# Kernel tuning notes

Hardware: AMD Instinct MI355X
Metric: run time of the kernel (lower is better)

## Reference

```python
import jax, jax.numpy as jnp
import numpy as np

N_NODES = 50000
N_EDGES = 800000
IN_DIM = 128
HID_DIM = 128
OUT_DIM = 128


def setup_inputs() -> dict:
    key = jax.random.key(0)
    k = jax.random.split(key, 8)
    x = jax.random.normal(k[0], (N_NODES, IN_DIM), dtype=jnp.float32)
    edge_index = jax.random.randint(k[1], (2, N_EDGES), 0, N_NODES, dtype=jnp.int64)
    edge_weight = jax.random.uniform(k[2], (N_EDGES,), dtype=jnp.float32)
    # GCNConv params: weight [in, out] (glorot-ish), bias [out]
    W1 = jax.random.normal(k[3], (IN_DIM, HID_DIM), dtype=jnp.float32) / np.sqrt(IN_DIM)
    b1 = jnp.zeros((HID_DIM,), dtype=jnp.float32)
    W2 = jax.random.normal(k[4], (HID_DIM, OUT_DIM), dtype=jnp.float32) / np.sqrt(HID_DIM)
    b2 = jnp.zeros((OUT_DIM,), dtype=jnp.float32)
    return {"x": x, "edge_index": edge_index, "edge_weight": edge_weight,
            "W1": W1, "b1": b1, "W2": W2, "b2": b2}


def gcn_conv(x, W, b, src, dst, ew, n_nodes):
    """PyG GCNConv: add self-loops (weight 1), symmetric D^-1/2 (A+I) D^-1/2 norm."""
    h = x @ W  # [N, out]
    deg = jax.ops.segment_sum(ew, dst, num_segments=n_nodes) + 1.0  # +1 for self loop
    dis = jnp.where(deg > 0, jax.lax.rsqrt(deg), 0.0)  # deg^{-1/2}
    norm = dis[src] * ew * dis[dst]  # [E]
    msg = h[src] * norm[:, None]  # gather + weight -> [E, out]
    agg = jax.ops.segment_sum(msg, dst, num_segments=n_nodes)
    # self-loop contribution: norm_ii = dis[i] * 1 * dis[i]
    agg = agg + h * (dis * dis)[:, None]
    return agg + b


def reference(x, edge_index, edge_weight, W1, b1, W2, b2):
    src, dst = edge_index[0], edge_index[1]
    n = x.shape[0]
    h = gcn_conv(x, W1, b1, src, dst, edge_weight, n)
    h = jax.nn.relu(h)
    out = gcn_conv(h, W2, b2, src, dst, edge_weight, n)
    return out
```

## Files before the change

### kernel.cpp

```cpp
#include <hip/hip_runtime.h>

#define NDIM 128
#define NPART 8

typedef __attribute__((ext_vector_type(8))) short bf16x8;
typedef __attribute__((ext_vector_type(4))) float floatx4;

__device__ __forceinline__ float bflo(unsigned v){ return __uint_as_float(v << 16); }
__device__ __forceinline__ float bfhi(unsigned v){ return __uint_as_float(v & 0xffff0000u); }
__device__ __forceinline__ unsigned f2bf(float f){
  unsigned u = __float_as_uint(f);
  return (u + 0x7fffu + ((u >> 16) & 1u)) >> 16;
}

__global__ void k_prep0(unsigned long long* __restrict__ pk,
                        const float* __restrict__ W1, const float* __restrict__ W2,
                        unsigned short* __restrict__ Wp1, unsigned short* __restrict__ Wp2,
                        int n){
  int i = blockIdx.x * 256 + threadIdx.x;
  if (i < n) pk[i] = 0ULL;
  if (i < NDIM * NDIM){
    int k = i >> 7, c = i & 127;
    int kt = k >> 5, kq = (k >> 3) & 3, j = k & 7;
    int Lb = kq * 16 + (c & 15);
    int idx = (((kt * 8 + (c >> 4)) * 64) + Lb) * 8 + j;
    Wp1[idx] = (unsigned short)f2bf(W1[i]);
    Wp2[idx] = (unsigned short)f2bf(W2[i]);
  }
}

__global__ void k_deg(const int* __restrict__ ei, const float* __restrict__ ew,
                      unsigned long long* pk, unsigned short* __restrict__ rank, int E){
  int e = blockIdx.x * blockDim.x + threadIdx.x;
  if (e >= E) return;
  int d = ei[E + e];
  unsigned fx = (unsigned)__float2uint_rn(ew[e] * 1048576.0f);
  unsigned long long old = atomicAdd(&pk[d], (1ULL << 44) | (unsigned long long)fx);
  rank[e] = (unsigned short)(old >> 44);
}

__global__ __launch_bounds__(1024) void k_scan1(const unsigned long long* __restrict__ pk,
                                                int* __restrict__ off,
                                                int* __restrict__ bsum, int n){
  __shared__ int wsum[16];
  int t = threadIdx.x;
  int i = blockIdx.x * 1024 + t;
  int c = (i < n) ? (int)(pk[i] >> 44) : 0;
  int lane = t & 63, w = t >> 6;
  int v = c;
  #pragma unroll
  for (int d = 1; d < 64; d <<= 1){ int u = __shfl_up(v, d); if (lane >= d) v += u; }
  if (lane == 63) wsum[w] = v;
  __syncthreads();
  if (w == 0){
    int sv = (lane < 16) ? wsum[lane] : 0;
    #pragma unroll
    for (int d = 1; d < 16; d <<= 1){ int u = __shfl_up(sv, d); if (lane >= d) sv += u; }
    if (lane < 16) wsum[lane] = sv;
  }
  __syncthreads();
  int base = (w > 0) ? wsum[w - 1] : 0;
  if (i < n) off[i] = base + v - c;
  if (t == 1023) bsum[blockIdx.x] = wsum[15];
}

__global__ __launch_bounds__(1024) void k_scan23(int* __restrict__ off,
                                                 const int* __restrict__ bsum,
                                                 const unsigned long long* __restrict__ pk,
                                                 float* __restrict__ dis, int n, int E, int nb){
  __shared__ int sBase;
  int t = threadIdx.x;
  if (t < 64){
    int c2 = (t < nb) ? bsum[t] : 0;
    int v2 = c2;
    #pragma unroll
    for (int d = 1; d < 64; d <<= 1){ int u = __shfl_up(v2, d); if (t >= d) v2 += u; }
    if (t == (int)blockIdx.x) sBase = v2 - c2;
  }
  __syncthreads();
  int i = blockIdx.x * 1024 + t;
  if (i == 0) off[n] = E;
  if (i >= n) return;
  off[i] += sBase;
  float deg = 1.0f + (float)(pk[i] & ((1ULL << 44) - 1)) * (1.0f / 1048576.0f);
  dis[i] = rsqrtf(deg);
}

__global__ __launch_bounds__(256) void k_place(const int* __restrict__ ei,
                                               const float* __restrict__ ew,
                                               const unsigned short* __restrict__ rank,
                                               const float* __restrict__ dis,
                                               const int* __restrict__ off,
                                               unsigned* __restrict__ edges,
                                               int E, int N){
  int pid = blockIdx.x % NPART;
  int cid = blockIdx.x / NPART;
  int C   = gridDim.x / NPART;
  int per = (E + C - 1) / C;
  int e0 = cid * per;
  int e1 = min(e0 + per, E);
  int lo = (int)(((long long)pid * N) / NPART);
  int hi = (int)(((long long)(pid + 1) * N) / NPART);
  for (int e = e0 + threadIdx.x; e < e1; e += 256){
    int d = ei[E + e];
    if (d < lo || d >= hi) continue;
    int s = ei[e];
    float w = ew[e];
    int p = off[d] + (int)rank[e];
    edges[p] = (f2bf(dis[s] * w * dis[d]) << 16) | (unsigned)s;
  }
}

template<int XF32>
__global__ __launch_bounds__(256) void k_gemm_mfma(const void* __restrict__ Xv,
                                                   const unsigned short* __restrict__ Wp,
                                                   unsigned short* __restrict__ Hout,
                                                   int ntiles){
  __shared__ unsigned short Wb[4 * 8 * 64 * 8];
  int tid = threadIdx.x;
  for (int t = tid; t < 2048; t += 256)
    ((uint4*)Wb)[t] = ((const uint4*)Wp)[t];
  __syncthreads();

  int w = tid >> 6, L = tid & 63;
  int m = L & 15, q = L >> 4;
  for (int tile = blockIdx.x * 4 + w; tile < ntiles; tile += gridDim.x * 4){
    size_t row = (size_t)tile * 16 + m;
    floatx4 acc[8] = {};
    #pragma unroll
    for (int kt = 0; kt < 4; ++kt){
      bf16x8 a;
      if (XF32){
        const float* xp = (const float*)Xv + row * NDIM + kt * 32 + q * 8;
        float4 a0 = *(const float4*)xp;
        float4 a1 = *(const float4*)(xp + 4);
        unsigned short* as = (unsigned short*)&a;
        as[0] = f2bf(a0.x); as[1] = f2bf(a0.y); as[2] = f2bf(a0.z); as[3] = f2bf(a0.w);
        as[4] = f2bf(a1.x); as[5] = f2bf(a1.y); as[6] = f2bf(a1.z); as[7] = f2bf(a1.w);
      } else {
        a = *(const bf16x8*)((const unsigned short*)Xv + row * NDIM + kt * 32 + q * 8);
      }
      #pragma unroll
      for (int ct = 0; ct < 8; ++ct){
        bf16x8 b = *(const bf16x8*)&Wb[((kt * 8 + ct) * 64 + L) * 8];
        acc[ct] = __builtin_amdgcn_mfma_f32_16x16x32_bf16(a, b, acc[ct], 0, 0, 0);
      }
    }
    #pragma unroll
    for (int ct = 0; ct < 8; ++ct){
      #pragma unroll
      for (int r = 0; r < 4; ++r){
        size_t orow = (size_t)tile * 16 + q * 4 + r;
        Hout[orow * NDIM + ct * 16 + m] = (unsigned short)f2bf(acc[ct][r]);
      }
    }
  }
}

template<int OUT_F32>
__global__ __launch_bounds__(256) void k_agg(const unsigned short* __restrict__ H,
                                             const int* __restrict__ off,
                                             const unsigned* __restrict__ edges,
                                             const float* __restrict__ dis,
                                             const float* __restrict__ bias,
                                             void* __restrict__ out,
                                             int n, int do_relu){
  int g = threadIdx.x >> 6, L = threadIdx.x & 63;
  int i = blockIdx.x * 4 + g;
  if (i >= n) return;
  float di = dis[i];
  float dii = di * di;
  float2 bv = ((const float2*)bias)[L];
  unsigned hv = ((const unsigned*)(H + (size_t)i * NDIM))[L];
  float acc0 = fmaf(bflo(hv), dii, bv.x);
  float acc1 = fmaf(bfhi(hv), dii, bv.y);
  int p  = __builtin_amdgcn_readfirstlane(off[i]);
  int p1 = __builtin_amdgcn_readfirstlane(off[i + 1]);
  const char* Hb = (const char*)H;
  unsigned L4 = (unsigned)L * 4u;

  while (p + 16 <= p1){
    unsigned e[16], h[16];
    #pragma unroll
    for (int j = 0; j < 16; ++j) e[j] = __builtin_amdgcn_readfirstlane(edges[p + j]);
    #pragma unroll
    for (int j = 0; j < 16; ++j)
      h[j] = *(const unsigned*)(Hb + (((size_t)(e[j] & 0xFFFFu)) << 8) + L4);
    #pragma unroll
    for (int j = 0; j < 16; ++j){
      float w = bfhi(e[j]);
      acc0 = fmaf(bflo(h[j]), w, acc0);
      acc1 = fmaf(bfhi(h[j]), w, acc1);
    }
    p += 16;
  }
  while (p + 4 <= p1){
    unsigned e[4], h[4];
    #pragma unroll
    for (int j = 0; j < 4; ++j) e[j] = __builtin_amdgcn_readfirstlane(edges[p + j]);
    #pragma unroll
    for (int j = 0; j < 4; ++j)
      h[j] = *(const unsigned*)(Hb + (((size_t)(e[j] & 0xFFFFu)) << 8) + L4);
    #pragma unroll
    for (int j = 0; j < 4; ++j){
      float w = bfhi(e[j]);
      acc0 = fmaf(bflo(h[j]), w, acc0);
      acc1 = fmaf(bfhi(h[j]), w, acc1);
    }
    p += 4;
  }
  for (; p < p1; ++p){
    unsigned e = __builtin_amdgcn_readfirstlane(edges[p]);
    unsigned h2 = *(const unsigned*)(Hb + (((size_t)(e & 0xFFFFu)) << 8) + L4);
    float w = bfhi(e);
    acc0 = fmaf(bflo(h2), w, acc0);
    acc1 = fmaf(bfhi(h2), w, acc1);
  }
  if (do_relu){ acc0 = fmaxf(acc0, 0.f); acc1 = fmaxf(acc1, 0.f); }
  if (OUT_F32){
    ((float2*)((float*)out + (size_t)i * NDIM))[L] = make_float2(acc0, acc1);
  } else {
    ((unsigned*)((unsigned short*)out + (size_t)i * NDIM))[L] = (f2bf(acc1) << 16) | f2bf(acc0);
  }
}

extern "C" void kernel_launch(void* const* d_in, const int* in_sizes, int n_in,
                              void* d_out, int out_size, void* d_ws, size_t ws_size,
                              hipStream_t stream){
  const float* x  = (const float*)d_in[0];
  const int*   ei = (const int*)  d_in[1];
  const float* ew = (const float*)d_in[2];
  const float* W1 = (const float*)d_in[3];
  const float* b1 = (const float*)d_in[4];
  const float* W2 = (const float*)d_in[5];
  const float* b2 = (const float*)d_in[6];
  float* out = (float*)d_out;
  int N = in_sizes[0] / NDIM;
  int E = in_sizes[2];
  int nb = (N + 1023) / 1024;
  int ntiles = N / 16;

  char* p = (char*)d_ws;
  auto alloc = [&](size_t b) -> char* { char* r = p; p += (b + 255) & ~(size_t)255; return r; };
  unsigned long long* pk = (unsigned long long*)alloc((size_t)N * 8);
  float*    dis   = (float*)   alloc((size_t)N * 4);
  int*      off   = (int*)     alloc((size_t)(N + 1) * 4);
  int*      bsum  = (int*)     alloc((size_t)64 * 4);
  unsigned short* rank = (unsigned short*)alloc((size_t)E * 2);
  unsigned short* Wp1 = (unsigned short*)alloc(NDIM * NDIM * 2);
  unsigned short* Wp2 = (unsigned short*)alloc(NDIM * NDIM * 2);
  unsigned* edges = (unsigned*)alloc((size_t)E * 4);
  unsigned short* R = (unsigned short*)alloc((size_t)N * NDIM * 2);
  unsigned short* H1 = (unsigned short*)d_out;

  k_prep0<<<(N + 255) / 256, 256, 0, stream>>>(pk, W1, W2, Wp1, Wp2, N);
  k_deg  <<<(E + 255) / 256, 256, 0, stream>>>(ei, ew, pk, rank, E);
  k_scan1<<<nb, 1024, 0, stream>>>(pk, off, bsum, N);
  k_scan23<<<nb, 1024, 0, stream>>>(off, bsum, pk, dis, N, E, nb);
  k_place<<<NPART * 96, 256, 0, stream>>>(ei, ew, rank, dis, off, edges, E, N);

  int gg = (ntiles + 3) / 4;
  k_gemm_mfma<1><<<gg, 256, 0, stream>>>(x, Wp1, H1, ntiles);
  k_agg<0> <<<(N + 3) / 4, 256, 0, stream>>>(H1, off, edges, dis, b1, R, N, 1);
  k_gemm_mfma<0><<<gg, 256, 0, stream>>>(R, Wp2, R, ntiles);
  k_agg<1> <<<(N + 3) / 4, 256, 0, stream>>>(R, off, edges, dis, b2, out, N, 0);
}
```

Baseline: 238.5 us.

## Fuse first GEMM with degree kernel and pack weights inside GEMM blocks

Merges the layer-1 GEMM and the degree/rank atomic kernel into a single launch, with block ranges picking which body to run, so the compute-bound GEMM overlaps the atomic-bound degree pass. Weight conversion to packed bf16 now happens per block in shared memory, which removes the prep kernel and its packed-weight buffers but repeats the conversion in every block. It also gives k_place more blocks, writes layer-2 GEMM output to a separate buffer instead of in place, and unrolls the aggregation tail with an 8-edge step. GG is hardcoded to 782 blocks, which ties the GEMM grid to this node count.

```diff
diff --git a/kernel.cpp b/kernel.cpp
--- a/kernel.cpp
+++ b/kernel.cpp
@@ -2,6 +2,7 @@
 
 #define NDIM 128
 #define NPART 8
+#define GG 782
 
 typedef __attribute__((ext_vector_type(8))) short bf16x8;
 typedef __attribute__((ext_vector_type(4))) float floatx4;
@@ -13,30 +14,93 @@
   return (u + 0x7fffu + ((u >> 16) & 1u)) >> 16;
 }
 
-__global__ void k_prep0(unsigned long long* __restrict__ pk,
-                        const float* __restrict__ W1, const float* __restrict__ W2,
-                        unsigned short* __restrict__ Wp1, unsigned short* __restrict__ Wp2,
-                        int n){
+__global__ void k_zero(unsigned long long* __restrict__ pk, int n){
   int i = blockIdx.x * 256 + threadIdx.x;
   if (i < n) pk[i] = 0ULL;
-  if (i < NDIM * NDIM){
-    int k = i >> 7, c = i & 127;
+}
+
+template<int XF32>
+__device__ __forceinline__ void gemm_body(const void* __restrict__ Xv,
+                                          const float* __restrict__ W,
+                                          unsigned short* __restrict__ Hout,
+                                          int ntiles, int bid){
+  __shared__ unsigned short Wb[4 * 8 * 64 * 8];
+  int tid = threadIdx.x;
+  for (int t = tid; t < NDIM * NDIM; t += 256){
+    int k = t >> 7, c = t & 127;
     int kt = k >> 5, kq = (k >> 3) & 3, j = k & 7;
-    int Lb = kq * 16 + (c & 15);
-    int idx = (((kt * 8 + (c >> 4)) * 64) + Lb) * 8 + j;
-    Wp1[idx] = (unsigned short)f2bf(W1[i]);
-    Wp2[idx] = (unsigned short)f2bf(W2[i]);
-  }
-}
-
-__global__ void k_deg(const int* __restrict__ ei, const float* __restrict__ ew,
-                      unsigned long long* pk, unsigned short* __restrict__ rank, int E){
-  int e = blockIdx.x * blockDim.x + threadIdx.x;
+    Wb[(((kt * 8 + (c >> 4)) * 64) + kq * 16 + (c & 15)) * 8 + j] =
+        (unsigned short)f2bf(W[t]);
+  }
+  __syncthreads();
+
+  int w = tid >> 6, L = tid & 63;
+  int m = L & 15, q = L >> 4;
+  for (int tile = bid * 4 + w; tile < ntiles; tile += GG * 4){
+    size_t row = (size_t)tile * 16 + m;
+    floatx4 acc[8] = {};
+    #pragma unroll
+    for (int kt = 0; kt < 4; ++kt){
+      bf16x8 a;
+      if (XF32){
+        const float* xp = (const float*)Xv + row * NDIM + kt * 32 + q * 8;
+        float4 a0 = *(const float4*)xp;
+        float4 a1 = *(const float4*)(xp + 4);
+        unsigned short* as = (unsigned short*)&a;
+        as[0] = f2bf(a0.x); as[1] = f2bf(a0.y); as[2] = f2bf(a0.z); as[3] = f2bf(a0.w);
+        as[4] = f2bf(a1.x); as[5] = f2bf(a1.y); as[6] = f2bf(a1.z); as[7] = f2bf(a1.w);
+      } else {
+        a = *(const bf16x8*)((const unsigned short*)Xv + row * NDIM + kt * 32 + q * 8);
+      }
+      #pragma unroll
+      for (int ct = 0; ct < 8; ++ct){
+        bf16x8 b = *(const bf16x8*)&Wb[((kt * 8 + ct) * 64 + L) * 8];
+        acc[ct] = __builtin_amdgcn_mfma_f32_16x16x32_bf16(a, b, acc[ct], 0, 0, 0);
+      }
+    }
+    #pragma unroll
+    for (int ct = 0; ct < 8; ++ct){
+      #pragma unroll
+      for (int r = 0; r < 4; ++r){
+        size_t orow = (size_t)tile * 16 + q * 4 + r;
+        Hout[orow * NDIM + ct * 16 + m] = (unsigned short)f2bf(acc[ct][r]);
+      }
+    }
+  }
+}
+
+__device__ __forceinline__ void deg_body(const int* __restrict__ ei,
+                                         const float* __restrict__ ew,
+                                         unsigned long long* pk,
+                                         unsigned short* __restrict__ rank,
+                                         int E, int bid){
+  int e = bid * 256 + threadIdx.x;
   if (e >= E) return;
   int d = ei[E + e];
   unsigned fx = (unsigned)__float2uint_rn(ew[e] * 1048576.0f);
   unsigned long long old = atomicAdd(&pk[d], (1ULL << 44) | (unsigned long long)fx);
   rank[e] = (unsigned short)(old >> 44);
+}
+
+__global__ __launch_bounds__(256) void k_union(const float* __restrict__ x,
+                                               const float* __restrict__ W1,
+                                               unsigned short* __restrict__ H1,
+                                               int ntiles,
+                                               const int* __restrict__ ei,
+                                               const float* __restrict__ ew,
+                                               unsigned long long* pk,
+                                               unsigned short* __restrict__ rank,
+                                               int E){
+  int bid = blockIdx.x;
+  if (bid < GG) gemm_body<1>(x, W1, H1, ntiles, bid);
+  else          deg_body(ei, ew, pk, rank, E, bid - GG);
+}
+
+__global__ __launch_bounds__(256) void k_gemm2(const void* __restrict__ Xv,
+                                               const float* __restrict__ W,
+                                               unsigned short* __restrict__ Hout,
+                                               int ntiles){
+  gemm_body<0>(Xv, W, Hout, ntiles, blockIdx.x);
 }
 
 __global__ __launch_bounds__(1024) void k_scan1(const unsigned long long* __restrict__ pk,
@@ -111,52 +175,6 @@
   }
 }
 
-template<int XF32>
-__global__ __launch_bounds__(256) void k_gemm_mfma(const void* __restrict__ Xv,
-                                                   const unsigned short* __restrict__ Wp,
-                                                   unsigned short* __restrict__ Hout,
-                                                   int ntiles){
-  __shared__ unsigned short Wb[4 * 8 * 64 * 8];
-  int tid = threadIdx.x;
-  for (int t = tid; t < 2048; t += 256)
-    ((uint4*)Wb)[t] = ((const uint4*)Wp)[t];
-  __syncthreads();
-
-  int w = tid >> 6, L = tid & 63;
-  int m = L & 15, q = L >> 4;
-  for (int tile = blockIdx.x * 4 + w; tile < ntiles; tile += gridDim.x * 4){
-    size_t row = (size_t)tile * 16 + m;
-    floatx4 acc[8] = {};
-    #pragma unroll
-    for (int kt = 0; kt < 4; ++kt){
-      bf16x8 a;
-      if (XF32){
-        const float* xp = (const float*)Xv + row * NDIM + kt * 32 + q * 8;
-        float4 a0 = *(const float4*)xp;
-        float4 a1 = *(const float4*)(xp + 4);
-        unsigned short* as = (unsigned short*)&a;
-        as[0] = f2bf(a0.x); as[1] = f2bf(a0.y); as[2] = f2bf(a0.z); as[3] = f2bf(a0.w);
-        as[4] = f2bf(a1.x); as[5] = f2bf(a1.y); as[6] = f2bf(a1.z); as[7] = f2bf(a1.w);
-      } else {
-        a = *(const bf16x8*)((const unsigned short*)Xv + row * NDIM + kt * 32 + q * 8);
-      }
-      #pragma unroll
-      for (int ct = 0; ct < 8; ++ct){
-        bf16x8 b = *(const bf16x8*)&Wb[((kt * 8 + ct) * 64 + L) * 8];
-        acc[ct] = __builtin_amdgcn_mfma_f32_16x16x32_bf16(a, b, acc[ct], 0, 0, 0);
-      }
-    }
-    #pragma unroll
-    for (int ct = 0; ct < 8; ++ct){
-      #pragma unroll
-      for (int r = 0; r < 4; ++r){
-        size_t orow = (size_t)tile * 16 + q * 4 + r;
-        Hout[orow * NDIM + ct * 16 + m] = (unsigned short)f2bf(acc[ct][r]);
-      }
-    }
-  }
-}
-
 template<int OUT_F32>
 __global__ __launch_bounds__(256) void k_agg(const unsigned short* __restrict__ H,
                                              const int* __restrict__ off,
@@ -194,7 +212,22 @@
     }
     p += 16;
   }
-  while (p + 4 <= p1){
+  if (p + 8 <= p1){
+    unsigned e[8], h[8];
+    #pragma unroll
+    for (int j = 0; j < 8; ++j) e[j] = __builtin_amdgcn_readfirstlane(edges[p + j]);
+    #pragma unroll
+    for (int j = 0; j < 8; ++j)
+      h[j] = *(const unsigned*)(Hb + (((size_t)(e[j] & 0xFFFFu)) << 8) + L4);
+    #pragma unroll
+    for (int j = 0; j < 8; ++j){
+      float w = bfhi(e[j]);
+      acc0 = fmaf(bflo(h[j]), w, acc0);
+      acc1 = fmaf(bfhi(h[j]), w, acc1);
+    }
+    p += 8;
+  }
+  if (p + 4 <= p1){
     unsigned e[4], h[4];
     #pragma unroll
     for (int j = 0; j < 4; ++j) e[j] = __builtin_amdgcn_readfirstlane(edges[p + j]);
@@ -247,21 +280,19 @@
   int*      off   = (int*)     alloc((size_t)(N + 1) * 4);
   int*      bsum  = (int*)     alloc((size_t)64 * 4);
   unsigned short* rank = (unsigned short*)alloc((size_t)E * 2);
-  unsigned short* Wp1 = (unsigned short*)alloc(NDIM * NDIM * 2);
-  unsigned short* Wp2 = (unsigned short*)alloc(NDIM * NDIM * 2);
   unsigned* edges = (unsigned*)alloc((size_t)E * 4);
-  unsigned short* R = (unsigned short*)alloc((size_t)N * NDIM * 2);
+  unsigned short* R  = (unsigned short*)alloc((size_t)N * NDIM * 2);
+  unsigned short* H2 = (unsigned short*)alloc((size_t)N * NDIM * 2);
   unsigned short* H1 = (unsigned short*)d_out;
 
-  k_prep0<<<(N + 255) / 256, 256, 0, stream>>>(pk, W1, W2, Wp1, Wp2, N);
-  k_deg  <<<(E + 255) / 256, 256, 0, stream>>>(ei, ew, pk, rank, E);
+  int degB = (E + 255) / 256;
+  k_zero <<<(N + 255) / 256, 256, 0, stream>>>(pk, N);
+  k_union<<<GG + degB, 256, 0, stream>>>(x, W1, H1, ntiles, ei, ew, pk, rank, E);
   k_scan1<<<nb, 1024, 0, stream>>>(pk, off, bsum, N);
   k_scan23<<<nb, 1024, 0, stream>>>(off, bsum, pk, dis, N, E, nb);
-  k_place<<<NPART * 96, 256, 0, stream>>>(ei, ew, rank, dis, off, edges, E, N);
-
-  int gg = (ntiles + 3) / 4;
-  k_gemm_mfma<1><<<gg, 256, 0, stream>>>(x, Wp1, H1, ntiles);
+  k_place<<<NPART * 256, 256, 0, stream>>>(ei, ew, rank, dis, off, edges, E, N);
+
   k_agg<0> <<<(N + 3) / 4, 256, 0, stream>>>(H1, off, edges, dis, b1, R, N, 1);
-  k_gemm_mfma<0><<<gg, 256, 0, stream>>>(R, Wp2, R, ntiles);
-  k_agg<1> <<<(N + 3) / 4, 256, 0, stream>>>(R, off, edges, dis, b2, out, N, 0);
-}
+  k_gemm2<<<GG, 256, 0, stream>>>(R, W2, H2, ntiles);
+  k_agg<1> <<<(N + 3) / 4, 256, 0, stream>>>(H2, off, edges, dis, b2, out, N, 0);
+}
```

Measured after the change: 233.3 us. -2.2%, faster.

## Use half-wave per node in aggregation with 8-byte gathers; enlarge place grid

Applied to the files above, without the earlier changes.

The aggregation kernel now assigns 32 lanes per node instead of a full 64-lane wavefront. Each lane gathers 8 bytes (four bf16 features) per neighbour and keeps four accumulators, so two nodes are processed per wave. Edge indices are read as per-lane loads instead of readfirstlane, and the remainder handling is restructured into 8/4/1 steps. The edge placement kernel gets more blocks, and the second GEMM writes to a separate buffer instead of operating in place. This aims to raise memory-level parallelism and cut wave count in the gather-bound aggregation, at the cost of divergence between the two half-waves when their node degrees differ.

```diff
diff --git a/kernel.cpp b/kernel.cpp
--- a/kernel.cpp
+++ b/kernel.cpp
@@ -165,62 +165,99 @@
                                              const float* __restrict__ bias,
                                              void* __restrict__ out,
                                              int n, int do_relu){
-  int g = threadIdx.x >> 6, L = threadIdx.x & 63;
-  int i = blockIdx.x * 4 + g;
+  int w  = threadIdx.x >> 6;
+  int hf = (threadIdx.x >> 5) & 1;
+  int l  = threadIdx.x & 31;
+  int i = blockIdx.x * 8 + w * 2 + hf;
   if (i >= n) return;
   float di = dis[i];
   float dii = di * di;
-  float2 bv = ((const float2*)bias)[L];
-  unsigned hv = ((const unsigned*)(H + (size_t)i * NDIM))[L];
-  float acc0 = fmaf(bflo(hv), dii, bv.x);
-  float acc1 = fmaf(bfhi(hv), dii, bv.y);
-  int p  = __builtin_amdgcn_readfirstlane(off[i]);
-  int p1 = __builtin_amdgcn_readfirstlane(off[i + 1]);
+  float4 bv = ((const float4*)bias)[l];
+  unsigned long long hv = ((const unsigned long long*)(H + (size_t)i * NDIM))[l];
+  unsigned hv0 = (unsigned)hv, hv1 = (unsigned)(hv >> 32);
+  float acc0 = fmaf(bflo(hv0), dii, bv.x);
+  float acc1 = fmaf(bfhi(hv0), dii, bv.y);
+  float acc2 = fmaf(bflo(hv1), dii, bv.z);
+  float acc3 = fmaf(bfhi(hv1), dii, bv.w);
+  int p  = off[i];
+  int p1 = off[i + 1];
   const char* Hb = (const char*)H;
-  unsigned L4 = (unsigned)L * 4u;
+  unsigned L8 = (unsigned)l * 8u;
 
   while (p + 16 <= p1){
-    unsigned e[16], h[16];
-    #pragma unroll
-    for (int j = 0; j < 16; ++j) e[j] = __builtin_amdgcn_readfirstlane(edges[p + j]);
+    unsigned e[16]; unsigned long long h[16];
+    #pragma unroll
+    for (int j = 0; j < 16; ++j) e[j] = edges[p + j];
     #pragma unroll
     for (int j = 0; j < 16; ++j)
-      h[j] = *(const unsigned*)(Hb + (((size_t)(e[j] & 0xFFFFu)) << 8) + L4);
+      h[j] = *(const unsigned long long*)(Hb + (((size_t)(e[j] & 0xFFFFu)) << 8) + L8);
     #pragma unroll
     for (int j = 0; j < 16; ++j){
-      float w = bfhi(e[j]);
-      acc0 = fmaf(bflo(h[j]), w, acc0);
-      acc1 = fmaf(bfhi(h[j]), w, acc1);
+      float wt = bfhi(e[j]);
+      unsigned lo = (unsigned)h[j], hi = (unsigned)(h[j] >> 32);
+      acc0 = fmaf(bflo(lo), wt, acc0);
+      acc1 = fmaf(bfhi(lo), wt, acc1);
+      acc2 = fmaf(bflo(hi), wt, acc2);
+      acc3 = fmaf(bfhi(hi), wt, acc3);
     }
     p += 16;
   }
-  while (p + 4 <= p1){
-    unsigned e[4], h[4];
-    #pragma unroll
-    for (int j = 0; j < 4; ++j) e[j] = __builtin_amdgcn_readfirstlane(edges[p + j]);
+  if (p + 8 <= p1){
+    unsigned e[8]; unsigned long long h[8];
+    #pragma unroll
+    for (int j = 0; j < 8; ++j) e[j] = edges[p + j];
+    #pragma unroll
+    for (int j = 0; j < 8; ++j)
+      h[j] = *(const unsigned long long*)(Hb + (((size_t)(e[j] & 0xFFFFu)) << 8) + L8);
+    #pragma unroll
+    for (int j = 0; j < 8; ++j){
+      float wt = bfhi(e[j]);
+      unsigned lo = (unsigned)h[j], hi = (unsigned)(h[j] >> 32);
+      acc0 = fmaf(bflo(lo), wt, acc0);
+      acc1 = fmaf(bfhi(lo), wt, acc1);
+      acc2 = fmaf(bflo(hi), wt, acc2);
+      acc3 = fmaf(bfhi(hi), wt, acc3);
+    }
+    p += 8;
+  }
+  if (p + 4 <= p1){
+    unsigned e[4]; unsigned long long h[4];
+    #pragma unroll
+    for (int j = 0; j < 4; ++j) e[j] = edges[p + j];
     #pragma unroll
     for (int j = 0; j < 4; ++j)
-      h[j] = *(const unsigned*)(Hb + (((size_t)(e[j] & 0xFFFFu)) << 8) + L4);
+      h[j] = *(const unsigned long long*)(Hb + (((size_t)(e[j] & 0xFFFFu)) << 8) + L8);
     #pragma unroll
     for (int j = 0; j < 4; ++j){
-      float w = bfhi(e[j]);
-      acc0 = fmaf(bflo(h[j]), w, acc0);
-      acc1 = fmaf(bfhi(h[j]), w, acc1);
+      float wt = bfhi(e[j]);
+      unsigned lo = (unsigned)h[j], hi = (unsigned)(h[j] >> 32);
+      acc0 = fmaf(bflo(lo), wt, acc0);
+      acc1 = fmaf(bfhi(lo), wt, acc1);
+      acc2 = fmaf(bflo(hi), wt, acc2);
+      acc3 = fmaf(bfhi(hi), wt, acc3);
     }
     p += 4;
   }
   for (; p < p1; ++p){
-    unsigned e = __builtin_amdgcn_readfirstlane(edges[p]);
-    unsigned h2 = *(const unsigned*)(Hb + (((size_t)(e & 0xFFFFu)) << 8) + L4);
-    float w = bfhi(e);
-    acc0 = fmaf(bflo(h2), w, acc0);
-    acc1 = fmaf(bfhi(h2), w, acc1);
-  }
-  if (do_relu){ acc0 = fmaxf(acc0, 0.f); acc1 = fmaxf(acc1, 0.f); }
+    unsigned e = edges[p];
+    unsigned long long h2 = *(const unsigned long long*)(Hb + (((size_t)(e & 0xFFFFu)) << 8) + L8);
+    float wt = bfhi(e);
+    unsigned lo = (unsigned)h2, hi = (unsigned)(h2 >> 32);
+    acc0 = fmaf(bflo(lo), wt, acc0);
+    acc1 = fmaf(bfhi(lo), wt, acc1);
+    acc2 = fmaf(bflo(hi), wt, acc2);
+    acc3 = fmaf(bfhi(hi), wt, acc3);
+  }
+  if (do_relu){
+    acc0 = fmaxf(acc0, 0.f); acc1 = fmaxf(acc1, 0.f);
+    acc2 = fmaxf(acc2, 0.f); acc3 = fmaxf(acc3, 0.f);
+  }
   if (OUT_F32){
-    ((float2*)((float*)out + (size_t)i * NDIM))[L] = make_float2(acc0, acc1);
+    ((float4*)((float*)out + (size_t)i * NDIM))[l] = make_float4(acc0, acc1, acc2, acc3);
   } else {
-    ((unsigned*)((unsigned short*)out + (size_t)i * NDIM))[L] = (f2bf(acc1) << 16) | f2bf(acc0);
+    unsigned lo = (f2bf(acc1) << 16) | f2bf(acc0);
+    unsigned hi = (f2bf(acc3) << 16) | f2bf(acc2);
+    ((uint2*)((unsigned short*)out + (size_t)i * NDIM))[l] = make_uint2(lo, hi);
   }
 }
 
@@ -250,18 +287,19 @@
   unsigned short* Wp1 = (unsigned short*)alloc(NDIM * NDIM * 2);
   unsigned short* Wp2 = (unsigned short*)alloc(NDIM * NDIM * 2);
   unsigned* edges = (unsigned*)alloc((size_t)E * 4);
-  unsigned short* R = (unsigned short*)alloc((size_t)N * NDIM * 2);
+  unsigned short* R  = (unsigned short*)alloc((size_t)N * NDIM * 2);
+  unsigned short* H2 = (unsigned short*)alloc((size_t)N * NDIM * 2);
   unsigned short* H1 = (unsigned short*)d_out;
 
   k_prep0<<<(N + 255) / 256, 256, 0, stream>>>(pk, W1, W2, Wp1, Wp2, N);
   k_deg  <<<(E + 255) / 256, 256, 0, stream>>>(ei, ew, pk, rank, E);
   k_scan1<<<nb, 1024, 0, stream>>>(pk, off, bsum, N);
   k_scan23<<<nb, 1024, 0, stream>>>(off, bsum, pk, dis, N, E, nb);
-  k_place<<<NPART * 96, 256, 0, stream>>>(ei, ew, rank, dis, off, edges, E, N);
+  k_place<<<NPART * 256, 256, 0, stream>>>(ei, ew, rank, dis, off, edges, E, N);
 
   int gg = (ntiles + 3) / 4;
   k_gemm_mfma<1><<<gg, 256, 0, stream>>>(x, Wp1, H1, ntiles);
-  k_agg<0> <<<(N + 3) / 4, 256, 0, stream>>>(H1, off, edges, dis, b1, R, N, 1);
-  k_gemm_mfma<0><<<gg, 256, 0, stream>>>(R, Wp2, R, ntiles);
-  k_agg<1> <<<(N + 3) / 4, 256, 0, stream>>>(R, off, edges, dis, b2, out, N, 0);
-}
+  k_agg<0> <<<(N + 7) / 8, 256, 0, stream>>>(H1, off, edges, dis, b1, R, N, 1);
+  k_gemm_mfma<0><<<gg, 256, 0, stream>>>(R, Wp2, H2, ntiles);
+  k_agg<1> <<<(N + 7) / 8, 256, 0, stream>>>(H2, off, edges, dis, b2, out, N, 0);
+}
```

Result: slower. 244.3 us (+2.5%).
